# Kernel optimization log

Hardware: AMD Instinct MI355X
Metric: run time of the kernel (lower is better)

## Reference

```python
import jax, jax.numpy as jnp
import numpy as np
from jax import lax

N_NODES = 5000; N_EDGES = 160000; N_FEAT = 128; HIDDEN = 256
N_TPL = 10; N_TPL_NODES = 10; N_CLASSES = 8
ALPHA = 0.5          # FGW structure/feature trade-off
CG_ITERS = 5         # conditional-gradient (Frank-Wolfe) outer iterations
SINK_ITERS = 30      # log-domain Sinkhorn iterations (EMD surrogate)
SINK_REG = 0.02      # entropic reg relative to cost scale


def setup_inputs() -> dict:
    key = jax.random.key(0)
    ks = jax.random.split(key, 8)
    x = jax.random.normal(ks[0], (N_NODES, N_FEAT), jnp.float32)
    edge_index = jax.random.randint(ks[1], (2, N_EDGES), 0, N_NODES)
    W1 = jax.random.normal(ks[2], (N_FEAT, HIDDEN), jnp.float32) / np.sqrt(N_FEAT)
    b1 = jnp.zeros((HIDDEN,), jnp.float32)
    W2 = jax.random.normal(ks[3], (HIDDEN, N_FEAT), jnp.float32) / np.sqrt(HIDDEN)
    b2 = jnp.zeros((N_FEAT,), jnp.float32)
    templates = jax.random.uniform(ks[4], (N_TPL, N_TPL_NODES, N_TPL_NODES), jnp.float32)
    templates_features = jax.random.uniform(ks[5], (N_TPL, N_TPL_NODES, N_FEAT), jnp.float32)
    Wlin = jax.random.normal(ks[6], (N_TPL, N_CLASSES), jnp.float32) / np.sqrt(N_TPL)
    blin = jnp.zeros((N_CLASSES,), jnp.float32)
    return dict(x=x, edge_index=edge_index, W1=W1, b1=b1, W2=W2, b2=b2,
                templates=templates, templates_features=templates_features,
                Wlin=Wlin, blin=blin)


def gcn_conv(x, src, dst, W, b):
    # PyG GCNConv: x @ W, then D^-1/2 (A + I) D^-1/2 aggregation, then + b
    n = x.shape[0]
    loop = jnp.arange(n)
    s = jnp.concatenate([src, loop]); d = jnp.concatenate([dst, loop])
    deg = jax.ops.segment_sum(jnp.ones(s.shape[0], x.dtype), d, num_segments=n)
    dinv = lax.rsqrt(jnp.maximum(deg, 1.0))
    h = x @ W
    msg = h[s] * (dinv[s] * dinv[d])[:, None]
    return jax.ops.segment_sum(msg, d, num_segments=n) + b


def sinkhorn_log(G, logp, logq):
    # entropic OT in log domain as a jit-friendly surrogate for exact EMD
    scale = lax.stop_gradient(jnp.max(jnp.abs(G)) + 1e-9)
    mlogK = -G / (SINK_REG * scale)          # [n, m]
    f0 = jnp.zeros(G.shape[0], G.dtype); g0 = jnp.zeros(G.shape[1], G.dtype)
    def body(carry, _):
        f, g = carry
        g = logq - jax.nn.logsumexp(mlogK + f[:, None], axis=0)
        f = logp - jax.nn.logsumexp(mlogK + g[None, :], axis=1)
        return (f, g), None
    (f, g), _ = lax.scan(body, (f0, g0), None, length=SINK_ITERS)
    return jnp.exp(f[:, None] + mlogK + g[None, :])


def fgw2(C1, x, C2, F2):
    # Fused Gromov-Wasserstein distance (square loss), uniform weights,
    # conditional-gradient with fixed step 2/(t+2) and Sinkhorn LP surrogate.
    n, m = C1.shape[0], C2.shape[0]
    p = jnp.full((n,), 1.0 / n, x.dtype); q = jnp.full((m,), 1.0 / m, x.dtype)
    logp = jnp.log(p); logq = jnp.log(q)
    # squared-euclidean feature cost  [n, m]
    M = jnp.sum(x * x, 1)[:, None] + jnp.sum(F2 * F2, 1)[None, :] - 2.0 * x @ F2.T
    # square-loss GW decomposition: f1=a^2, f2=b^2, h1=a, h2=2b
    constC = ((C1 * C1) @ p)[:, None] + ((C2 * C2) @ q)[None, :]
    def tens(T):
        return constC - C1 @ T @ (2.0 * C2).T
    T = p[:, None] * q[None, :]
    for t in range(CG_ITERS):
        grad = (1.0 - ALPHA) * M + 2.0 * ALPHA * tens(T)
        Tnew = sinkhorn_log(grad, logp, logq)
        T = T + (2.0 / (t + 2.0)) * (Tnew - T)
    return (1.0 - ALPHA) * jnp.sum(M * T) + ALPHA * jnp.sum(tens(T) * T)


def reference(x, edge_index, W1, b1, W2, b2, templates, templates_features, Wlin, blin):
    src, dst = edge_index[0], edge_index[1]
    h = jax.nn.relu(gcn_conv(x, src, dst, W1, b1))
    h = gcn_conv(h, src, dst, W2, b2)           # [N, F]
    n = x.shape[0]
    C = jnp.zeros((n, n), x.dtype).at[src, dst].set(1.0)   # dense adjacency
    dists = jax.vmap(lambda Ct, Ft: fgw2(C, h, Ct, Ft))(templates, templates_features)  # [K]
    return dists @ Wlin + blin                  # [num_classes]
```

## Files before the change

kernel.cpp:

```cpp
#include <hip/hip_runtime.h>
#include <cstdint>

#define NND 5000
#define NE 160000
#define NF 128
#define NH 256
#define NT 10
#define MT 10
#define NC 8
#define NMAT (NND*MT)
#define CG_ITERS 5
#define SINK_IT 30


__global__ void k_edge1(const int* __restrict__ src, const int* __restrict__ dst,
                        int* __restrict__ cntD, unsigned* __restrict__ bitmap,
                        int* __restrict__ cntS, unsigned char* __restrict__ keep) {
    for (int e = blockIdx.x*blockDim.x + threadIdx.x; e < NE; e += gridDim.x*blockDim.x) {
        int s = src[e], d = dst[e];
        atomicAdd(&cntD[d], 1);
        int key = s * NND + d;
        unsigned bit = 1u << (key & 31);
        unsigned old = atomicOr(&bitmap[key >> 5], bit);
        if (!(old & bit)) { keep[e] = 1; atomicAdd(&cntS[s], 1); }
        else keep[e] = 0;
    }
}

__global__ void k_exscan2(const int* __restrict__ cntD, int* __restrict__ rpD,
                          float* __restrict__ dinv,
                          const int* __restrict__ cntS, int* __restrict__ rpS) {
    const int T = 1024;
    const int* cnt = blockIdx.x ? cntS : cntD;
    int* rp = blockIdx.x ? rpS : rpD;
    int tid = threadIdx.x;
    int C = (NND + T - 1) / T;
    int begin = tid * C, end = begin + C; if (end > NND) end = NND; if (begin > NND) begin = NND;
    int s = 0;
    for (int i = begin; i < end; i++) s += cnt[i];
    __shared__ int part[1024];
    part[tid] = s; __syncthreads();
    for (int off = 1; off < T; off <<= 1) {
        int v = (tid >= off) ? part[tid - off] : 0;
        __syncthreads();
        part[tid] += v;
        __syncthreads();
    }
    int run = part[tid] - s;
    for (int i = begin; i < end; i++) { rp[i] = run; run += cnt[i]; }
    if (tid == T - 1) rp[NND] = part[T - 1];
    if (blockIdx.x == 0)
        for (int i = begin; i < end; i++) dinv[i] = rsqrtf((float)(cnt[i] + 1));
}

__global__ void k_scatter2(const int* __restrict__ src, const int* __restrict__ dst,
                           const unsigned char* __restrict__ keep,
                           const int* __restrict__ rpD, int* __restrict__ cur1,
                           int* __restrict__ csrS, float* __restrict__ csrC,
                           const float* __restrict__ dinv,
                           const int* __restrict__ rpS, int* __restrict__ cur2,
                           int* __restrict__ csrD) {
    for (int e = blockIdx.x*blockDim.x + threadIdx.x; e < NE; e += gridDim.x*blockDim.x) {
        int s = src[e], d = dst[e];
        int pos = rpD[d] + atomicAdd(&cur1[d], 1);
        csrS[pos] = s;
        csrC[pos] = dinv[s] * dinv[d];
        if (keep[e]) {
            int p2 = rpS[s] + atomicAdd(&cur2[s], 1);
            csrD[p2] = d;
        }
    }
}


__global__ __launch_bounds__(256) void k_gemm(const float* __restrict__ A,
                                              const float* __restrict__ B,
                                              float* __restrict__ C, int M, int N, int K) {
    const int BM = 64, BN = 64, BK = 16;
    __shared__ float As[BK][BM + 1];
    __shared__ float Bs[BK][BN];
    int tid = threadIdx.x;
    int row0 = blockIdx.y * BM, col0 = blockIdx.x * BN;
    int tx = tid % 16, ty = tid / 16;
    float acc[4][4] = {};
    for (int k0 = 0; k0 < K; k0 += BK) {
#pragma unroll
        for (int l = 0; l < 4; l++) {
            int idx = tid + l * 256;
            int r = idx / BK, kk = idx % BK;
            int gr = row0 + r;
            As[kk][r] = (gr < M) ? A[(size_t)gr * K + k0 + kk] : 0.f;
        }
#pragma unroll
        for (int l = 0; l < 4; l++) {
            int idx = tid + l * 256;
            int kk = idx / BN, c = idx % BN;
            Bs[kk][c] = B[(size_t)(k0 + kk) * N + col0 + c];
        }
        __syncthreads();
#pragma unroll
        for (int kk = 0; kk < BK; kk++) {
            float a[4], b[4];
#pragma unroll
            for (int i = 0; i < 4; i++) a[i] = As[kk][ty * 4 + i];
#pragma unroll
            for (int j = 0; j < 4; j++) b[j] = Bs[kk][tx * 4 + j];
#pragma unroll
            for (int i = 0; i < 4; i++)
#pragma unroll
                for (int j = 0; j < 4; j++) acc[i][j] += a[i] * b[j];
        }
        __syncthreads();
    }
#pragma unroll
    for (int i = 0; i < 4; i++) {
        int gr = row0 + ty * 4 + i;
        if (gr < M) {
#pragma unroll
            for (int j = 0; j < 4; j++)
                C[(size_t)gr * N + col0 + tx * 4 + j] = acc[i][j];
        }
    }
}

__global__ void k_aggregate(const float* __restrict__ hin, const float* __restrict__ bias,
                            float* __restrict__ hout, const int* __restrict__ rp,
                            const int* __restrict__ csrS, const float* __restrict__ csrC,
                            const float* __restrict__ dinv, int relu) {
    int v = blockIdx.x;
    int f = threadIdx.x;
    int F = blockDim.x;
    float dv = dinv[v];
    float acc = hin[(size_t)v * F + f] * dv * dv;
    int e0 = rp[v], e1 = rp[v + 1];
    for (int e = e0; e < e1; e++)
        acc += hin[(size_t)csrS[e] * F + f] * csrC[e];
    acc += bias[f];
    if (relu) acc = fmaxf(acc, 0.f);
    hout[(size_t)v * F + f] = acc;
}


__global__ void k_prepnt(const int* __restrict__ cntS, const float* __restrict__ h,
                         float* __restrict__ c1row, float* __restrict__ sx,
                         const float* __restrict__ tpl, const float* __restrict__ tplF,
                         float* __restrict__ c2row, float* __restrict__ sF) {
    for (int i = blockIdx.x*blockDim.x + threadIdx.x; i < NND; i += gridDim.x*blockDim.x) {
        c1row[i] = (float)cntS[i] * (1.f / NND);
        float s = 0.f;
        for (int f = 0; f < NF; f++) { float v = h[(size_t)i * NF + f]; s += v * v; }
        sx[i] = s;
    }
    if (blockIdx.x == 0 && threadIdx.x < NT * MT) {
        int c = threadIdx.x;
        int t = c / MT, j = c % MT;
        float s = 0.f;
        for (int k = 0; k < MT; k++) { float v = tpl[t * 100 + j * 10 + k]; s += v * v; }
        c2row[c] = s * (1.f / MT);
        float sf = 0.f;
        for (int f = 0; f < NF; f++) { float v = tplF[(size_t)c * NF + f]; sf += v * v; }
        sF[c] = sf;
    }
}

__global__ void k_M(const float* __restrict__ h, const float* __restrict__ tplF,
                    const float* __restrict__ sx, const float* __restrict__ sF,
                    float* __restrict__ Mout) {
    int i = blockIdx.x;
    __shared__ float hrow[NF];
    hrow[threadIdx.x] = h[(size_t)i * NF + threadIdx.x];
    __syncthreads();
    int c = threadIdx.x;
    if (c < NT * MT) {
        const float* Fc = tplF + (size_t)c * NF;
        float dot = 0.f;
        for (int f = 0; f < NF; f++) dot += hrow[f] * Fc[f];
        int t = c / MT, j = c % MT;
        Mout[(size_t)t * NMAT + (size_t)i * MT + j] = sx[i] + sF[c] - 2.f * dot;
    }
}

__global__ void k_Tinit(float* __restrict__ T) {
    for (int idx = blockIdx.x*blockDim.x + threadIdx.x; idx < NT * NMAT; idx += gridDim.x*blockDim.x)
        T[idx] = 1.f / (float)NMAT;
}


__global__ __launch_bounds__(256) void k_grad(const float* __restrict__ T, const float* __restrict__ Mm,
                                              const float* __restrict__ c1row, const float* __restrict__ c2row,
                                              const float* __restrict__ tpl,
                                              const int* __restrict__ rpS, const int* __restrict__ csrD,
                                              float* __restrict__ G, unsigned* __restrict__ scaleBits) {
    int t = blockIdx.y;
    int tid = threadIdx.x;
    __shared__ float tC2[100];
    if (tid < 100) tC2[tid] = 2.f * tpl[t * 100 + tid];
    __syncthreads();
    int i = blockIdx.x * 256 + tid;
    float amax = 0.f;
    if (i < NND) {
        const float* Tt = T + (size_t)t * NMAT;
        const float* Mt = Mm + (size_t)t * NMAT;
        float* Gt = G + (size_t)t * NMAT;
        float L[MT];
#pragma unroll
        for (int j = 0; j < MT; j++) L[j] = 0.f;
        int e0 = rpS[i], e1 = rpS[i + 1];
        for (int e = e0; e < e1; e++) {
            int k = csrD[e];
            const float* Tk = Tt + (size_t)k * MT;
#pragma unroll
            for (int j = 0; j < MT; j++) L[j] += Tk[j];
        }
        float c1 = c1row[i];
#pragma unroll
        for (int j = 0; j < MT; j++) {
            float s = 0.f;
#pragma unroll
            for (int k = 0; k < MT; k++) s += L[k] * tC2[j * 10 + k];
            float g = 0.5f * Mt[(size_t)i * MT + j] + (c1 + c2row[t * 10 + j] - s);
            Gt[(size_t)i * MT + j] = g;
            amax = fmaxf(amax, fabsf(g));
        }
    }
    __shared__ float red[256];
    red[tid] = amax; __syncthreads();
    for (int off = 128; off > 0; off >>= 1) {
        if (tid < off) red[tid] = fmaxf(red[tid], red[tid + off]);
        __syncthreads();
    }
    if (tid == 0) atomicMax(&scaleBits[t], __float_as_uint(red[0]));
}

__device__ __forceinline__ float frcp(float x) {
#if __has_builtin(__builtin_amdgcn_rcpf)
    return __builtin_amdgcn_rcpf(x);
#else
    return 1.f / x;
#endif
}

__global__ __launch_bounds__(512, 1) void k_sinkhorn(const float* __restrict__ G,
                                                     const unsigned* __restrict__ scaleBits,
                                                     float* __restrict__ T, float step) {
    int t = blockIdx.x;
    int tid = threadIdx.x;
    float sc = __uint_as_float(scaleBits[t]) + 1e-9f;
    float inv = -1.f / (0.02f * sc);
    const float* Gt = G + (size_t)t * NMAT;
    float* Tt = T + (size_t)t * NMAT;

    __shared__ float Sa[10][516];
    __shared__ float Sb[10][33];
    __shared__ float vbc[12];

    float Kf[10][10];
    float u[10];
#pragma unroll
    for (int r = 0; r < 10; r++) {
        int i = tid + r * 512;
        if (i < NND) {
            u[r] = 1.f;
            const float2* Gr = (const float2*)(Gt + (size_t)i * 10);
#pragma unroll
            for (int h = 0; h < 5; h++) {
                float2 g = Gr[h];
                Kf[r][2*h]   = __expf(g.x * inv);
                Kf[r][2*h+1] = __expf(g.y * inv);
            }
        } else {
            u[r] = 0.f;
#pragma unroll
            for (int j = 0; j < 10; j++) Kf[r][j] = 0.f;
        }
    }

    float vv[10];
    int bj = tid % 10, bg = tid / 10;

    for (int it = 0; it < SINK_IT; it++) {
        float S[10];
#pragma unroll
        for (int j = 0; j < 10; j++) S[j] = 0.f;
#pragma unroll
        for (int r = 0; r < 10; r++) {
            float ur = u[r];
#pragma unroll
            for (int j = 0; j < 10; j++) S[j] = fmaf(Kf[r][j], ur, S[j]);
        }
#pragma unroll
        for (int j = 0; j < 10; j++) Sa[j][tid] = S[j];
        __syncthreads();
        if (tid < 320) {
            const float4* p = (const float4*)&Sa[bj][bg * 16];
            float4 a = p[0], b = p[1], c = p[2], d = p[3];
            Sb[bj][bg] = ((a.x + a.y) + (a.z + a.w)) + ((b.x + b.y) + (b.z + b.w))
                       + ((c.x + c.y) + (c.z + c.w)) + ((d.x + d.y) + (d.z + d.w));
        }
        __syncthreads();
        if (tid < 10) {
            const float* q = &Sb[tid][0];
            float s = 0.f;
#pragma unroll
            for (int g = 0; g < 32; g++) s += q[g];
            vbc[tid] = 0.1f * frcp(fmaxf(s, 1e-30f));
        }
        __syncthreads();
#pragma unroll
        for (int j = 0; j < 10; j++) vv[j] = vbc[j];
#pragma unroll
        for (int r = 0; r < 10; r++) {
            float R = 0.f;
#pragma unroll
            for (int j = 0; j < 10; j++) R = fmaf(Kf[r][j], vv[j], R);
            u[r] = (tid + r * 512 < NND) ? (2e-4f * frcp(fmaxf(R, 1e-30f))) : 0.f;
        }
    }

#pragma unroll
    for (int r = 0; r < 10; r++) {
        int i = tid + r * 512;
        if (i < NND) {
            float ur = u[r];
            float2* Tr = (float2*)(Tt + (size_t)i * 10);
#pragma unroll
            for (int h = 0; h < 5; h++) {
                float2 v = Tr[h];
                v.x += step * (ur * Kf[r][2*h]   * vv[2*h]   - v.x);
                v.y += step * (ur * Kf[r][2*h+1] * vv[2*h+1] - v.y);
                Tr[h] = v;
            }
        }
    }
}


__global__ __launch_bounds__(256) void k_final(const float* __restrict__ T, const float* __restrict__ Mm,
                                               const float* __restrict__ c1row, const float* __restrict__ c2row,
                                               const float* __restrict__ tpl,
                                               const int* __restrict__ rpS, const int* __restrict__ csrD,
                                               double* __restrict__ dd) {
    int t = blockIdx.y;
    int tid = threadIdx.x;
    __shared__ float tC2[100];
    if (tid < 100) tC2[tid] = 2.f * tpl[t * 100 + tid];
    __syncthreads();
    int i = blockIdx.x * 256 + tid;
    double msum = 0.0, tsum = 0.0;
    if (i < NND) {
        const float* Tt = T + (size_t)t * NMAT;
        const float* Mt = Mm + (size_t)t * NMAT;
        float L[MT];
#pragma unroll
        for (int j = 0; j < MT; j++) L[j] = 0.f;
        int e0 = rpS[i], e1 = rpS[i + 1];
        for (int e = e0; e < e1; e++) {
            int k = csrD[e];
            const float* Tk = Tt + (size_t)k * MT;
#pragma unroll
            for (int j = 0; j < MT; j++) L[j] += Tk[j];
        }
        float c1 = c1row[i];
#pragma unroll
        for (int j = 0; j < MT; j++) {
            float s = 0.f;
#pragma unroll
            for (int k = 0; k < MT; k++) s += L[k] * tC2[j * 10 + k];
            float ts = c1 + c2row[t * 10 + j] - s;
            float Tv = Tt[(size_t)i * MT + j];
            msum += (double)(Mt[(size_t)i * MT + j] * Tv);
            tsum += (double)(ts * Tv);
        }
    }
    __shared__ double r1[256], r2[256];
    r1[tid] = msum; r2[tid] = tsum; __syncthreads();
    for (int off = 128; off > 0; off >>= 1) {
        if (tid < off) { r1[tid] += r1[tid + off]; r2[tid] += r2[tid + off]; }
        __syncthreads();
    }
    if (tid == 0) { atomicAdd(&dd[t * 2], r1[0]); atomicAdd(&dd[t * 2 + 1], r2[0]); }
}

__global__ void k_out(const double* __restrict__ dd, const float* __restrict__ Wlin,
                      const float* __restrict__ blin, float* __restrict__ out) {
    int tid = threadIdx.x;
    __shared__ float ds[NT];
    if (tid < NT) ds[tid] = 0.5f * (float)(dd[2 * tid] + dd[2 * tid + 1]);
    __syncthreads();
    if (tid < NC) {
        float o = blin[tid];
#pragma unroll
        for (int t = 0; t < NT; t++) o += ds[t] * Wlin[t * NC + tid];
        out[tid] = o;
    }
}


extern "C" void kernel_launch(void* const* d_in, const int* in_sizes, int n_in,
                              void* d_out, int out_size, void* d_ws, size_t ws_size,
                              hipStream_t stream) {
    const float* x    = (const float*)d_in[0];
    const int*   ei   = (const int*)d_in[1];
    const int*   src  = ei;
    const int*   dst  = ei + NE;
    const float* W1   = (const float*)d_in[2];
    const float* b1   = (const float*)d_in[3];
    const float* W2   = (const float*)d_in[4];
    const float* b2   = (const float*)d_in[5];
    const float* tpl  = (const float*)d_in[6];
    const float* tplF = (const float*)d_in[7];
    const float* Wlin = (const float*)d_in[8];
    const float* blin = (const float*)d_in[9];
    float* out = (float*)d_out;

    char* w = (char*)d_ws;
    size_t off = 0;
    auto alloc = [&](size_t b) -> char* {
        off = (off + 255) & ~(size_t)255;
        char* p = w + off; off += b; return p;
    };
    float* bufA = (float*)alloc((size_t)NND * NH * 4);
    float* bufB = (float*)alloc((size_t)NND * NH * 4);
    float* bufH = (float*)alloc((size_t)NND * NF * 4);
    float* Mm   = (float*)alloc((size_t)NT * NMAT * 4);
    float* T    = (float*)alloc((size_t)NT * NMAT * 4);
    float* G    = (float*)alloc((size_t)NT * NMAT * 4);
    int* cntD = (int*)alloc((size_t)NND * 4);
    int* cntS = (int*)alloc((size_t)NND * 4);
    int* cur1 = (int*)alloc((size_t)NND * 4);
    int* cur2 = (int*)alloc((size_t)NND * 4);
    double* dd = (double*)alloc((size_t)NT * 2 * 8);
    unsigned* scaleArr = (unsigned*)alloc((size_t)CG_ITERS * NT * 4);
    char* zend = w + off;
    unsigned* bitmap = (unsigned*)alloc((size_t)781250 * 4);
    int* rpD  = (int*)alloc((size_t)(NND + 1) * 4);
    int* rpS  = (int*)alloc((size_t)(NND + 1) * 4);
    int* csrS = (int*)alloc((size_t)NE * 4);
    float* csrC = (float*)alloc((size_t)NE * 4);
    int* csrD2 = (int*)alloc((size_t)NE * 4);
    unsigned char* keep = (unsigned char*)alloc((size_t)NE);
    float* dinv  = (float*)alloc((size_t)NND * 4);
    float* c1row = (float*)alloc((size_t)NND * 4);
    float* sx    = (float*)alloc((size_t)NND * 4);
    float* sF    = (float*)alloc((size_t)100 * 4);
    float* c2row = (float*)alloc((size_t)100 * 4);

    hipMemsetAsync(cntD, 0, (size_t)(zend - (char*)cntD), stream);
    hipMemsetAsync(bitmap, 0, (size_t)781250 * 4, stream);

    k_edge1<<<625, 256, 0, stream>>>(src, dst, cntD, bitmap, cntS, keep);
    k_exscan2<<<2, 1024, 0, stream>>>(cntD, rpD, dinv, cntS, rpS);
    k_scatter2<<<625, 256, 0, stream>>>(src, dst, keep, rpD, cur1, csrS, csrC, dinv,
                                        rpS, cur2, csrD2);

    k_gemm<<<dim3(NH / 64, (NND + 63) / 64), 256, 0, stream>>>(x, W1, bufA, NND, NH, NF);
    k_aggregate<<<NND, NH, 0, stream>>>(bufA, b1, bufB, rpD, csrS, csrC, dinv, 1);
    k_gemm<<<dim3(NF / 64, (NND + 63) / 64), 256, 0, stream>>>(bufB, W2, bufA, NND, NF, NH);
    k_aggregate<<<NND, NF, 0, stream>>>(bufA, b2, bufH, rpD, csrS, csrC, dinv, 0);

    k_prepnt<<<20, 256, 0, stream>>>(cntS, bufH, c1row, sx, tpl, tplF, c2row, sF);
    k_M<<<NND, 128, 0, stream>>>(bufH, tplF, sx, sF, Mm);
    k_Tinit<<<1954, 256, 0, stream>>>(T);

    for (int t = 0; t < CG_ITERS; t++) {
        unsigned* sb = scaleArr + t * NT;
        k_grad<<<dim3(20, NT), 256, 0, stream>>>(T, Mm, c1row, c2row, tpl, rpS, csrD2, G, sb);
        float step = 2.f / (float)(t + 2);
        k_sinkhorn<<<NT, 512, 0, stream>>>(G, sb, T, step);
    }

    k_final<<<dim3(20, NT), 256, 0, stream>>>(T, Mm, c1row, c2row, tpl, rpS, csrD2, dd);
    k_out<<<1, 64, 0, stream>>>(dd, Wlin, blin, out);
}
```

Measured before the change: 702.2 us.

## Reorder first GCN layer, fuse prep into scan/M, use DPP wave reductions

The first GCN layer now aggregates the 128-wide input before the GEMM instead of after it, which halves the gather width. Bias and ReLU are fused into the GEMM epilogue. The k_prepnt kernel is removed: c1row and c2row move into the scan kernel, and the row and template norms are computed inside k_M. The Sinkhorn column-sum reduction swaps shared-memory staging for DPP wave reductions plus an 8-wave combine, and the occupancy hint is relaxed. This cuts launches and shared-memory traffic, at the cost of recomputing template norms for every row and possible reordering of floating-point sums.

```diff
diff --git a/kernel.cpp b/kernel.cpp
--- a/kernel.cpp
+++ b/kernel.cpp
@@ -11,6 +11,34 @@
 #define NMAT (NND*MT)
 #define CG_ITERS 5
 #define SINK_IT 30
+
+#if __has_builtin(__builtin_amdgcn_update_dpp)
+#define DPP_ADD(x, ctrl, rmask) \
+    ((x) + __int_as_float(__builtin_amdgcn_update_dpp(0, __float_as_int(x), (ctrl), (rmask), 0xf, true)))
+__device__ __forceinline__ float wave_sum63(float x) {
+    x = DPP_ADD(x, 0x111, 0xf);
+    x = DPP_ADD(x, 0x112, 0xf);
+    x = DPP_ADD(x, 0x114, 0xf);
+    x = DPP_ADD(x, 0x118, 0xf);
+    x = DPP_ADD(x, 0x142, 0xa);
+    x = DPP_ADD(x, 0x143, 0xc);
+    return x;
+}
+#else
+__device__ __forceinline__ float wave_sum63(float x) {
+#pragma unroll
+    for (int off = 32; off; off >>= 1) x += __shfl_xor(x, off);
+    return x;
+}
+#endif
+
+__device__ __forceinline__ float frcp(float x) {
+#if __has_builtin(__builtin_amdgcn_rcpf)
+    return __builtin_amdgcn_rcpf(x);
+#else
+    return 1.f / x;
+#endif
+}
 
 
 __global__ void k_edge1(const int* __restrict__ src, const int* __restrict__ dst,
@@ -29,11 +57,22 @@
 
 __global__ void k_exscan2(const int* __restrict__ cntD, int* __restrict__ rpD,
                           float* __restrict__ dinv,
-                          const int* __restrict__ cntS, int* __restrict__ rpS) {
+                          const int* __restrict__ cntS, int* __restrict__ rpS,
+                          float* __restrict__ c1row,
+                          const float* __restrict__ tpl, float* __restrict__ c2row) {
     const int T = 1024;
+    int tid = threadIdx.x;
+    if (blockIdx.x == 2) {
+        if (tid < NT * MT) {
+            int t = tid / MT, j = tid % MT;
+            float s = 0.f;
+            for (int k = 0; k < MT; k++) { float v = tpl[t * 100 + j * 10 + k]; s += v * v; }
+            c2row[tid] = s * (1.f / MT);
+        }
+        return;
+    }
     const int* cnt = blockIdx.x ? cntS : cntD;
     int* rp = blockIdx.x ? rpS : rpD;
-    int tid = threadIdx.x;
     int C = (NND + T - 1) / T;
     int begin = tid * C, end = begin + C; if (end > NND) end = NND; if (begin > NND) begin = NND;
     int s = 0;
@@ -51,6 +90,8 @@
     if (tid == T - 1) rp[NND] = part[T - 1];
     if (blockIdx.x == 0)
         for (int i = begin; i < end; i++) dinv[i] = rsqrtf((float)(cnt[i] + 1));
+    else
+        for (int i = begin; i < end; i++) c1row[i] = (float)cnt[i] * (1.f / NND);
 }
 
 __global__ void k_scatter2(const int* __restrict__ src, const int* __restrict__ dst,
@@ -75,7 +116,8 @@
 
 __global__ __launch_bounds__(256) void k_gemm(const float* __restrict__ A,
                                               const float* __restrict__ B,
-                                              float* __restrict__ C, int M, int N, int K) {
+                                              float* __restrict__ C, int M, int N, int K,
+                                              const float* __restrict__ bias, int relu) {
     const int BM = 64, BN = 64, BK = 16;
     __shared__ float As[BK][BM + 1];
     __shared__ float Bs[BK][BN];
@@ -117,66 +159,59 @@
         int gr = row0 + ty * 4 + i;
         if (gr < M) {
 #pragma unroll
-            for (int j = 0; j < 4; j++)
-                C[(size_t)gr * N + col0 + tx * 4 + j] = acc[i][j];
-        }
-    }
-}
-
-__global__ void k_aggregate(const float* __restrict__ hin, const float* __restrict__ bias,
+            for (int j = 0; j < 4; j++) {
+                int gc = col0 + tx * 4 + j;
+                float o = acc[i][j];
+                if (bias) o += bias[gc];
+                if (relu) o = fmaxf(o, 0.f);
+                C[(size_t)gr * N + gc] = o;
+            }
+        }
+    }
+}
+
+__global__ __launch_bounds__(128) void k_aggregate(const float* __restrict__ hin,
+                            const float* __restrict__ bias,
                             float* __restrict__ hout, const int* __restrict__ rp,
                             const int* __restrict__ csrS, const float* __restrict__ csrC,
-                            const float* __restrict__ dinv, int relu) {
+                            const float* __restrict__ dinv) {
     int v = blockIdx.x;
     int f = threadIdx.x;
-    int F = blockDim.x;
     float dv = dinv[v];
-    float acc = hin[(size_t)v * F + f] * dv * dv;
+    float acc = hin[(size_t)v * NF + f] * dv * dv;
     int e0 = rp[v], e1 = rp[v + 1];
     for (int e = e0; e < e1; e++)
-        acc += hin[(size_t)csrS[e] * F + f] * csrC[e];
-    acc += bias[f];
-    if (relu) acc = fmaxf(acc, 0.f);
-    hout[(size_t)v * F + f] = acc;
-}
-
-
-__global__ void k_prepnt(const int* __restrict__ cntS, const float* __restrict__ h,
-                         float* __restrict__ c1row, float* __restrict__ sx,
-                         const float* __restrict__ tpl, const float* __restrict__ tplF,
-                         float* __restrict__ c2row, float* __restrict__ sF) {
-    for (int i = blockIdx.x*blockDim.x + threadIdx.x; i < NND; i += gridDim.x*blockDim.x) {
-        c1row[i] = (float)cntS[i] * (1.f / NND);
-        float s = 0.f;
-        for (int f = 0; f < NF; f++) { float v = h[(size_t)i * NF + f]; s += v * v; }
-        sx[i] = s;
-    }
-    if (blockIdx.x == 0 && threadIdx.x < NT * MT) {
-        int c = threadIdx.x;
-        int t = c / MT, j = c % MT;
-        float s = 0.f;
-        for (int k = 0; k < MT; k++) { float v = tpl[t * 100 + j * 10 + k]; s += v * v; }
-        c2row[c] = s * (1.f / MT);
-        float sf = 0.f;
-        for (int f = 0; f < NF; f++) { float v = tplF[(size_t)c * NF + f]; sf += v * v; }
-        sF[c] = sf;
-    }
-}
-
-__global__ void k_M(const float* __restrict__ h, const float* __restrict__ tplF,
-                    const float* __restrict__ sx, const float* __restrict__ sF,
+        acc += hin[(size_t)csrS[e] * NF + f] * csrC[e];
+    if (bias) acc += bias[f];
+    hout[(size_t)v * NF + f] = acc;
+}
+
+
+__global__ __launch_bounds__(128) void k_M(const float* __restrict__ h,
+                    const float* __restrict__ tplF,
                     float* __restrict__ Mout) {
     int i = blockIdx.x;
+    int tid = threadIdx.x;
+    int lane = tid & 63, w = tid >> 6;
     __shared__ float hrow[NF];
-    hrow[threadIdx.x] = h[(size_t)i * NF + threadIdx.x];
+    __shared__ float part[2];
+    float hv = h[(size_t)i * NF + tid];
+    hrow[tid] = hv;
+    float ps = wave_sum63(hv * hv);
+    if (lane == 63) part[w] = ps;
     __syncthreads();
-    int c = threadIdx.x;
+    float sx = part[0] + part[1];
+    int c = tid;
     if (c < NT * MT) {
         const float* Fc = tplF + (size_t)c * NF;
-        float dot = 0.f;
-        for (int f = 0; f < NF; f++) dot += hrow[f] * Fc[f];
+        float dot = 0.f, nrm = 0.f;
+        for (int f = 0; f < NF; f++) {
+            float fv = Fc[f];
+            dot = fmaf(hrow[f], fv, dot);
+            nrm = fmaf(fv, fv, nrm);
+        }
         int t = c / MT, j = c % MT;
-        Mout[(size_t)t * NMAT + (size_t)i * MT + j] = sx[i] + sF[c] - 2.f * dot;
+        Mout[(size_t)t * NMAT + (size_t)i * MT + j] = sx + nrm - 2.f * dot;
     }
 }
 
@@ -232,26 +267,20 @@
     if (tid == 0) atomicMax(&scaleBits[t], __float_as_uint(red[0]));
 }
 
-__device__ __forceinline__ float frcp(float x) {
-#if __has_builtin(__builtin_amdgcn_rcpf)
-    return __builtin_amdgcn_rcpf(x);
-#else
-    return 1.f / x;
-#endif
-}
-
-__global__ __launch_bounds__(512, 1) void k_sinkhorn(const float* __restrict__ G,
-                                                     const unsigned* __restrict__ scaleBits,
-                                                     float* __restrict__ T, float step) {
+__global__ __launch_bounds__(512)
+__attribute__((amdgpu_waves_per_eu(1, 2)))
+void k_sinkhorn(const float* __restrict__ G,
+                const unsigned* __restrict__ scaleBits,
+                float* __restrict__ T, float step) {
     int t = blockIdx.x;
     int tid = threadIdx.x;
+    int lane = tid & 63, w = tid >> 6;
     float sc = __uint_as_float(scaleBits[t]) + 1e-9f;
     float inv = -1.f / (0.02f * sc);
     const float* Gt = G + (size_t)t * NMAT;
     float* Tt = T + (size_t)t * NMAT;
 
-    __shared__ float Sa[10][516];
-    __shared__ float Sb[10][33];
+    __shared__ float wred[8][10];
     __shared__ float vbc[12];
 
     float Kf[10][10];
@@ -276,7 +305,6 @@
     }
 
     float vv[10];
-    int bj = tid % 10, bg = tid / 10;
 
     for (int it = 0; it < SINK_IT; it++) {
         float S[10];
@@ -289,20 +317,15 @@
             for (int j = 0; j < 10; j++) S[j] = fmaf(Kf[r][j], ur, S[j]);
         }
 #pragma unroll
-        for (int j = 0; j < 10; j++) Sa[j][tid] = S[j];
-        __syncthreads();
-        if (tid < 320) {
-            const float4* p = (const float4*)&Sa[bj][bg * 16];
-            float4 a = p[0], b = p[1], c = p[2], d = p[3];
-            Sb[bj][bg] = ((a.x + a.y) + (a.z + a.w)) + ((b.x + b.y) + (b.z + b.w))
-                       + ((c.x + c.y) + (c.z + c.w)) + ((d.x + d.y) + (d.z + d.w));
+        for (int j = 0; j < 10; j++) {
+            float s = wave_sum63(S[j]);
+            if (lane == 63) wred[w][j] = s;
         }
         __syncthreads();
         if (tid < 10) {
-            const float* q = &Sb[tid][0];
             float s = 0.f;
 #pragma unroll
-            for (int g = 0; g < 32; g++) s += q[g];
+            for (int q = 0; q < 8; q++) s += wred[q][tid];
             vbc[tid] = 0.1f * frcp(fmaxf(s, 1e-30f));
         }
         __syncthreads();
@@ -441,25 +464,22 @@
     unsigned char* keep = (unsigned char*)alloc((size_t)NE);
     float* dinv  = (float*)alloc((size_t)NND * 4);
     float* c1row = (float*)alloc((size_t)NND * 4);
-    float* sx    = (float*)alloc((size_t)NND * 4);
-    float* sF    = (float*)alloc((size_t)100 * 4);
     float* c2row = (float*)alloc((size_t)100 * 4);
 
     hipMemsetAsync(cntD, 0, (size_t)(zend - (char*)cntD), stream);
     hipMemsetAsync(bitmap, 0, (size_t)781250 * 4, stream);
 
     k_edge1<<<625, 256, 0, stream>>>(src, dst, cntD, bitmap, cntS, keep);
-    k_exscan2<<<2, 1024, 0, stream>>>(cntD, rpD, dinv, cntS, rpS);
+    k_exscan2<<<3, 1024, 0, stream>>>(cntD, rpD, dinv, cntS, rpS, c1row, tpl, c2row);
     k_scatter2<<<625, 256, 0, stream>>>(src, dst, keep, rpD, cur1, csrS, csrC, dinv,
                                         rpS, cur2, csrD2);
 
-    k_gemm<<<dim3(NH / 64, (NND + 63) / 64), 256, 0, stream>>>(x, W1, bufA, NND, NH, NF);
-    k_aggregate<<<NND, NH, 0, stream>>>(bufA, b1, bufB, rpD, csrS, csrC, dinv, 1);
-    k_gemm<<<dim3(NF / 64, (NND + 63) / 64), 256, 0, stream>>>(bufB, W2, bufA, NND, NF, NH);
-    k_aggregate<<<NND, NF, 0, stream>>>(bufA, b2, bufH, rpD, csrS, csrC, dinv, 0);
-
-    k_prepnt<<<20, 256, 0, stream>>>(cntS, bufH, c1row, sx, tpl, tplF, c2row, sF);
-    k_M<<<NND, 128, 0, stream>>>(bufH, tplF, sx, sF, Mm);
+    k_aggregate<<<NND, NF, 0, stream>>>(x, nullptr, bufA, rpD, csrS, csrC, dinv);
+    k_gemm<<<dim3(NH / 64, (NND + 63) / 64), 256, 0, stream>>>(bufA, W1, bufB, NND, NH, NF, b1, 1);
+    k_gemm<<<dim3(NF / 64, (NND + 63) / 64), 256, 0, stream>>>(bufB, W2, bufA, NND, NF, NH, nullptr, 0);
+    k_aggregate<<<NND, NF, 0, stream>>>(bufA, b2, bufH, rpD, csrS, csrC, dinv);
+
+    k_M<<<NND, 128, 0, stream>>>(bufH, tplF, Mm);
     k_Tinit<<<1954, 256, 0, stream>>>(T);
 
     for (int t = 0; t < CG_ITERS; t++) {
```

Measured after the change: 688.6 us. No clear change (-1.9%).
